# Kernel optimization log

Hardware: AMD Instinct MI355X
Metric: run time of the kernel (lower is better)

## Reference

```python
import jax, jax.numpy as jnp
import numpy as np

N, D_IN, D_OUT = 4096, 1024, 1024

def setup_inputs() -> dict:
    key = jax.random.key(0)
    k1, k2, k3, k4 = jax.random.split(key, 4)
    x = jax.random.normal(k1, (N, D_IN), dtype=jnp.float32)
    # original uses torch.rand (uniform [0,1)) for params
    w_query = jax.random.uniform(k2, (D_IN, D_OUT), dtype=jnp.float32)
    w_key = jax.random.uniform(k3, (D_IN, D_OUT), dtype=jnp.float32)
    w_value = jax.random.uniform(k4, (D_IN, D_OUT), dtype=jnp.float32)
    return {"x": x, "w_query": w_query, "w_key": w_key, "w_value": w_value}

def reference(x, w_query, w_key, w_value):
    queries = x @ w_query          # [N, d_out]
    keys = x @ w_key               # [N, d_out]
    values = x @ w_value           # [N, d_out]
    scale = keys.shape[-1] ** 0.5
    scores = queries @ keys.T      # [N, N]
    attn = jax.nn.softmax(scores / scale, axis=-1)
    return attn @ values           # [N, d_out]
```

## Files before the change

kernel.cpp:

```cpp
#include <hip/hip_runtime.h>
#include <math.h>

#define NROWS 4096
#define DDIM  1024

typedef __attribute__((ext_vector_type(8))) short short8;
typedef __attribute__((ext_vector_type(4))) float f32x4;

__device__ __forceinline__ ushort f2bf(float v) {
  union { float f; uint32_t u; } c; c.f = v;
  uint32_t u = c.u;
  uint32_t lsb = (u >> 16) & 1u;
  u += 0x7fffu + lsb;
  return (ushort)(u >> 16);
}
__device__ __forceinline__ float bf2f(ushort h) {
  union { uint32_t u; float f; } c; c.u = ((uint32_t)h) << 16;
  return c.f;
}

__device__ __forceinline__ void gll16(const void* g, void* l) {
  __builtin_amdgcn_global_load_lds((const __attribute__((address_space(1))) void*)g,
                                   (__attribute__((address_space(3))) void*)l, 16, 0, 0);
}

__device__ __forceinline__ size_t pidx(int r, int c, int ldt) {
  return ((size_t)((r >> 4) * ldt + (c >> 5))) * 512 +
         ((c >> 3) & 3) * 128 + (r & 15) * 8 + (c & 7);
}
__device__ __forceinline__ size_t pidxs(int r, int c, int ldt) {
  return ((size_t)((r >> 4) * ldt + (c >> 5))) * 1024 +
         ((c >> 3) & 3) * 128 + (r & 15) * 8 + (c & 7);
}

__global__ __launch_bounds__(256) void prep(const float* __restrict__ x,
                                            const float* __restrict__ wq,
                                            const float* __restrict__ wk,
                                            const float* __restrict__ wv,
                                            ushort* Xc,
                                            ushort* Wqc, ushort* Wkc, ushort* Wvh) {
  __shared__ float tl[32][33];
  const int b = blockIdx.x, t = threadIdx.x;
  if (b < 1024) {
    const f32x4* src = (const f32x4*)x;
#pragma unroll
    for (int r = 0; r < 4; ++r) {
      int i = b * 1024 + r * 256 + t;
      int row = i >> 8;
      int c = (i & 255) << 2;
      f32x4 v = __builtin_nontemporal_load(src + i);
      ushort4 h, l;
      h.x = f2bf(v.x); l.x = f2bf(v.x - bf2f(h.x));
      h.y = f2bf(v.y); l.y = f2bf(v.y - bf2f(h.y));
      h.z = f2bf(v.z); l.z = f2bf(v.z - bf2f(h.z));
      h.w = f2bf(v.w); l.w = f2bf(v.w - bf2f(h.w));
      size_t o = pidxs(row, c, DDIM / 32);
      *(ushort4*)(Xc + o) = h;
      *(ushort4*)(Xc + o + 512) = l;
    }
  } else {
    const int z = (b - 1024) >> 10;
    const int tile = (b - 1024) & 1023;
    const float* src = z == 0 ? wq : (z == 1 ? wk : wv);
    const int r0 = (tile >> 5) * 32;
    const int c0 = (tile & 31) * 32;
    const int tx = t & 31, ty = t >> 5;
    for (int i = ty; i < 32; i += 8)
      tl[i][tx] = __builtin_nontemporal_load(&src[(size_t)(r0 + i) * DDIM + c0 + tx]);
    __syncthreads();
    if (z == 2) {
      for (int i = ty; i < 32; i += 8) {
        float v = tl[tx][i];
        Wvh[pidx(c0 + i, r0 + tx, DDIM / 32)] = f2bf(v);
      }
    } else {
      ushort* d = z == 0 ? Wqc : Wkc;
      for (int i = ty; i < 32; i += 8) {
        float v = tl[tx][i];
        ushort h = f2bf(v);
        size_t o = pidxs(c0 + i, r0 + tx, DDIM / 32);
        d[o] = h;
        d[o + 512] = f2bf(v - bf2f(h));
      }
    }
  }
}

template <int MI, bool SPLIT, int KT, int SA, int SB>
__device__ __forceinline__ void direct_gemm(const ushort* __restrict__ A,
                                            const ushort* __restrict__ B,
                                            int m0, int n0, f32x4 (*acc)[4]) {
  const int t = threadIdx.x;
  const int wv = t >> 6, ln = t & 63;
  const int arb = (wv >> 1) * (MI * 16), crb = (wv & 1) * 64;
  const int ra = (m0 + arb) >> 4;
  const int rb = (n0 + crb) >> 4;

  uint oA[MI], oB[4];
#pragma unroll
  for (int i = 0; i < MI; ++i) oA[i] = (uint)(ra + i) * (uint)(KT * SA) + (uint)ln * 8u;
#pragma unroll
  for (int j = 0; j < 4; ++j) oB[j] = (uint)(rb + j) * (uint)(KT * SB) + (uint)ln * 8u;

  short8 ah0[MI], al0[MI], bh0[4], bl0[4];
  short8 ah1[MI], al1[MI], bh1[4], bl1[4];

#define DG_LOAD(sidx, AH, AL, BH, BL)                                        \
  {                                                                          \
    uint sa_ = (uint)(sidx) * (uint)SA;                                      \
    uint sb_ = (uint)(sidx) * (uint)SB;                                      \
    _Pragma("unroll") for (int i_ = 0; i_ < MI; ++i_) {                      \
      const ushort* pa_ = A + oA[i_] + sa_;                                  \
      AH[i_] = *(const short8*)pa_;                                          \
      if constexpr (SPLIT) AL[i_] = *(const short8*)(pa_ + 512);             \
    }                                                                        \
    _Pragma("unroll") for (int j_ = 0; j_ < 4; ++j_) {                       \
      const ushort* pb_ = B + oB[j_] + sb_;                                  \
      BH[j_] = *(const short8*)pb_;                                          \
      if constexpr (SPLIT) BL[j_] = *(const short8*)(pb_ + 512);             \
    }                                                                        \
  }

#define DG_MFMA(AH, AL, BH, BL)                                              \
  {                                                                          \
    __builtin_amdgcn_s_setprio(1);                                           \
    _Pragma("unroll") for (int j_ = 0; j_ < 4; ++j_) {                       \
      _Pragma("unroll") for (int i_ = 0; i_ < MI; ++i_) {                    \
        acc[i_][j_] = __builtin_amdgcn_mfma_f32_16x16x32_bf16(               \
            AH[i_], BH[j_], acc[i_][j_], 0, 0, 0);                           \
        if constexpr (SPLIT) {                                               \
          acc[i_][j_] = __builtin_amdgcn_mfma_f32_16x16x32_bf16(             \
              AH[i_], BL[j_], acc[i_][j_], 0, 0, 0);                         \
          acc[i_][j_] = __builtin_amdgcn_mfma_f32_16x16x32_bf16(             \
              AL[i_], BH[j_], acc[i_][j_], 0, 0, 0);                         \
        }                                                                    \
      }                                                                      \
    }                                                                        \
    __builtin_amdgcn_s_setprio(0);                                           \
  }

  DG_LOAD(0, ah0, al0, bh0, bl0);
#pragma unroll 1
  for (int s = 0; s < KT - 2; s += 2) {
    DG_LOAD(s + 1, ah1, al1, bh1, bl1);
    DG_MFMA(ah0, al0, bh0, bl0);
    DG_LOAD(s + 2, ah0, al0, bh0, bl0);
    DG_MFMA(ah1, al1, bh1, bl1);
  }
  DG_LOAD(KT - 1, ah1, al1, bh1, bl1);
  DG_MFMA(ah0, al0, bh0, bl0);
  DG_MFMA(ah1, al1, bh1, bl1);

#undef DG_LOAD
#undef DG_MFMA
}

__global__ __launch_bounds__(256) void gemm_qkv(const ushort* __restrict__ Xc,
                                                const ushort* __restrict__ Wqc,
                                                const ushort* __restrict__ Wkc,
                                                const ushort* __restrict__ Wvh,
                                                ushort* Qc, ushort* Kc, ushort* Vt) {
  const int id = blockIdx.y * 24 + blockIdx.x;
  const int wg = (id & 7) * 96 + (id >> 3);
  const int bx = wg % 24, by = wg / 24;
  const int which = bx % 3;
  const int g = bx / 3;
  const int t = threadIdx.x;
  const int wv = t >> 6, ln = t & 63;
  const int quad = ln >> 4, l16 = ln & 15;

  f32x4 acc[4][4];
#pragma unroll
  for (int i = 0; i < 4; ++i)
#pragma unroll
    for (int j = 0; j < 4; ++j) acc[i][j] = (f32x4){0.f, 0.f, 0.f, 0.f};

  if (which == 2) {
    const int m0 = g * 128;
    const int n0 = by * 128;
    direct_gemm<4, false, DDIM / 32, 512, 1024>(Wvh, Xc, m0, n0, acc);
#pragma unroll
    for (int i = 0; i < 4; ++i)
#pragma unroll
      for (int j = 0; j < 4; ++j) {
        int kv = n0 + (wv & 1) * 64 + j * 16 + l16;
        int d = m0 + (wv >> 1) * 64 + i * 16 + quad * 4;
#pragma unroll
        for (int r2 = 0; r2 < 4; ++r2)
          Vt[pidx(d + r2, kv, NROWS / 32)] = f2bf(acc[i][j][r2]);
      }
  } else {
    const int n0 = g * 128;
    const int m0 = by * 128;
    const ushort* Bc = which ? Wkc : Wqc;
    direct_gemm<4, true, DDIM / 32, 1024, 1024>(Xc, Bc, m0, n0, acc);
    const float scale = which ? 1.0f : 0.03125f;
    ushort* D = which ? Kc : Qc;
#pragma unroll
    for (int i = 0; i < 4; ++i)
#pragma unroll
      for (int j = 0; j < 4; ++j) {
        int col = n0 + (wv & 1) * 64 + j * 16 + l16;
        int rw = m0 + (wv >> 1) * 64 + i * 16 + quad * 4;
#pragma unroll
        for (int r2 = 0; r2 < 4; ++r2) {
          float v = acc[i][j][r2] * scale;
          ushort h = f2bf(v);
          size_t o = pidxs(rw + r2, col, DDIM / 32);
          D[o] = h;
          D[o + 512] = f2bf(v - bf2f(h));
        }
      }
  }
}

__global__ __launch_bounds__(512) void gemm_s(const ushort* __restrict__ Qc,
                                              const ushort* __restrict__ Kc,
                                              float* __restrict__ S) {
  __shared__ char smem[2][65536];
  const int bid = blockIdx.y * 16 + blockIdx.x;
  const int xcd = bid & 7, local = bid >> 3;
  const int m0 = ((xcd >> 1) * 4 + (local & 3)) * 256;
  const int n0 = ((xcd & 1) * 8 + (local >> 2)) * 256;
  const int t = threadIdx.x;
  const int w = t >> 6, ln = t & 63;
  const int wr = w >> 2, wc = w & 3;
  const int quad = ln >> 4, l16 = ln & 15;

  const char* srcBase = (w < 4)
      ? (const char*)Qc + (size_t)((m0 >> 4) + w * 4) * 65536
      : (const char*)Kc + (size_t)((n0 >> 4) + (w - 4) * 4) * 65536;
  srcBase += ln * 16;
  char* ldsBase = (char*)smem + w * 8192 + ln * 16;

  f32x4 acc[8][4];
#pragma unroll
  for (int i = 0; i < 8; ++i)
#pragma unroll
    for (int j = 0; j < 4; ++j) acc[i][j] = (f32x4){0.f, 0.f, 0.f, 0.f};

#pragma unroll
  for (int u = 0; u < 8; ++u)
    gll16(srcBase + (u >> 1) * 65536 + (u & 1) * 1024, ldsBase + u * 1024);
  asm volatile("s_waitcnt vmcnt(0)" ::: "memory");
  __builtin_amdgcn_s_barrier();

  const char* aB = (char*)smem + (wr * 8) * 2048 + ln * 16;
  const char* bB = (char*)smem + 32768 + (wc * 4) * 2048 + ln * 16;

#pragma unroll 1
  for (int kt = 0; kt < 32; ++kt) {
    const int cb = (kt & 1) << 16;
    const int nb = ((kt + 1) & 1) << 16;
    const char* srcK = srcBase + (size_t)(kt + 1) * 2048;

    if (kt < 31) {
#pragma unroll
      for (int u = 0; u < 8; ++u)
        gll16(srcK + (u >> 1) * 65536 + (u & 1) * 1024, ldsBase + nb + u * 1024);
    }

    short8 bh[4], bl[4];
#pragma unroll
    for (int j = 0; j < 4; ++j) {
      bh[j] = *(const short8*)(bB + cb + j * 2048);
      bl[j] = *(const short8*)(bB + cb + j * 2048 + 1024);
    }

#pragma unroll
    for (int p = 0; p < 4; ++p) {
      short8 ah0 = *(const short8*)(aB + cb + (2 * p) * 2048);
      short8 al0 = *(const short8*)(aB + cb + (2 * p) * 2048 + 1024);
      short8 ah1 = *(const short8*)(aB + cb + (2 * p + 1) * 2048);
      short8 al1 = *(const short8*)(aB + cb + (2 * p + 1) * 2048 + 1024);
      __builtin_amdgcn_s_setprio(1);
#pragma unroll
      for (int j_ = 0; j_ < 4; ++j_) {
        acc[2 * p][j_] = __builtin_amdgcn_mfma_f32_16x16x32_bf16(ah0, bh[j_], acc[2 * p][j_], 0, 0, 0);
        acc[2 * p][j_] = __builtin_amdgcn_mfma_f32_16x16x32_bf16(ah0, bl[j_], acc[2 * p][j_], 0, 0, 0);
        acc[2 * p][j_] = __builtin_amdgcn_mfma_f32_16x16x32_bf16(al0, bh[j_], acc[2 * p][j_], 0, 0, 0);
        acc[2 * p + 1][j_] = __builtin_amdgcn_mfma_f32_16x16x32_bf16(ah1, bh[j_], acc[2 * p + 1][j_], 0, 0, 0);
        acc[2 * p + 1][j_] = __builtin_amdgcn_mfma_f32_16x16x32_bf16(ah1, bl[j_], acc[2 * p + 1][j_], 0, 0, 0);
        acc[2 * p + 1][j_] = __builtin_amdgcn_mfma_f32_16x16x32_bf16(al1, bh[j_], acc[2 * p + 1][j_], 0, 0, 0);
      }
      __builtin_amdgcn_s_setprio(0);
    }

    asm volatile("s_waitcnt vmcnt(0)" ::: "memory");
    __builtin_amdgcn_s_barrier();
  }

#pragma unroll
  for (int i = 0; i < 8; ++i)
#pragma unroll
    for (int j = 0; j < 4; ++j) {
      int col = n0 + wc * 64 + j * 16 + l16;
      int rw = m0 + wr * 128 + i * 16 + quad * 4;
#pragma unroll
      for (int r2 = 0; r2 < 4; ++r2)
        S[(size_t)(rw + r2) * NROWS + col] = acc[i][j][r2];
    }
}

__global__ __launch_bounds__(256) void softmax_pack(const float* __restrict__ S,
                                                    ushort* __restrict__ P) {
  const int row = blockIdx.x, t = threadIdx.x;
  const float* Sr = S + (size_t)row * NROWS;
  const f32x4* S4 = (const f32x4*)Sr;
  f32x4 v[4];
  float mx = -3.4e38f;
#pragma unroll
  for (int c = 0; c < 4; ++c) {
    v[c] = S4[c * 256 + t];
    mx = fmaxf(mx, fmaxf(fmaxf(v[c].x, v[c].y), fmaxf(v[c].z, v[c].w)));
  }
  __shared__ float red[4];
  for (int o = 32; o >= 1; o >>= 1) mx = fmaxf(mx, __shfl_xor(mx, o));
  int wv = t >> 6, ln = t & 63;
  if (ln == 0) red[wv] = mx;
  __syncthreads();
  mx = fmaxf(fmaxf(red[0], red[1]), fmaxf(red[2], red[3]));
  float s = 0.f;
#pragma unroll
  for (int c = 0; c < 4; ++c) {
    v[c].x = __expf(v[c].x - mx);
    v[c].y = __expf(v[c].y - mx);
    v[c].z = __expf(v[c].z - mx);
    v[c].w = __expf(v[c].w - mx);
    s += v[c].x + v[c].y + v[c].z + v[c].w;
  }
  for (int o = 32; o >= 1; o >>= 1) s += __shfl_xor(s, o);
  __syncthreads();
  if (ln == 0) red[wv] = s;
  __syncthreads();
  s = red[0] + red[1] + red[2] + red[3];
  float inv = 1.f / s;
#pragma unroll
  for (int c = 0; c < 4; ++c) {
    ushort4 h;
    h.x = f2bf(v[c].x * inv);
    h.y = f2bf(v[c].y * inv);
    h.z = f2bf(v[c].z * inv);
    h.w = f2bf(v[c].w * inv);
    int c0 = 1024 * c + 4 * t;
    *(ushort4*)(P + pidx(row, c0, NROWS / 32)) = h;
  }
}

__global__ __launch_bounds__(256) void gemm_pv(const ushort* __restrict__ P,
                                               const ushort* __restrict__ Vt,
                                               float* __restrict__ Out) {
  const int n0 = blockIdx.x * 128, m0 = blockIdx.y * 128;
  const int t = threadIdx.x;
  const int wv = t >> 6, ln = t & 63;
  const int quad = ln >> 4, l16 = ln & 15;

  f32x4 acc[4][4];
#pragma unroll
  for (int i = 0; i < 4; ++i)
#pragma unroll
    for (int j = 0; j < 4; ++j) acc[i][j] = (f32x4){0.f, 0.f, 0.f, 0.f};

  direct_gemm<4, false, NROWS / 32, 512, 512>(P, Vt, m0, n0, acc);

#pragma unroll
  for (int i = 0; i < 4; ++i)
#pragma unroll
    for (int j = 0; j < 4; ++j) {
      int col = n0 + (wv & 1) * 64 + j * 16 + l16;
      int rw = m0 + (wv >> 1) * 64 + i * 16 + quad * 4;
#pragma unroll
      for (int r2 = 0; r2 < 4; ++r2)
        Out[(size_t)(rw + r2) * DDIM + col] = acc[i][j][r2];
    }
}

extern "C" void kernel_launch(void* const* d_in, const int* in_sizes, int n_in,
                              void* d_out, int out_size, void* d_ws, size_t ws_size,
                              hipStream_t stream) {
  const float* x  = (const float*)d_in[0];
  const float* wq = (const float*)d_in[1];
  const float* wk = (const float*)d_in[2];
  const float* wv = (const float*)d_in[3];
  char* ws = (char*)d_ws;
  const size_t MB = 1u << 20;

  ushort* Vt  = (ushort*)(ws + 0);
  ushort* Qc  = (ushort*)(ws + 8 * MB);
  ushort* Kc  = (ushort*)(ws + 24 * MB);
  ushort* Pp  = (ushort*)(ws + 8 * MB);
  ushort* Xc  = (ushort*)(ws + 40 * MB);
  ushort* Wqc = (ushort*)(ws + 56 * MB);
  ushort* Wkc = (ushort*)(ws + 60 * MB);
  ushort* Wvh = (ushort*)(ws + 64 * MB);
  float*  S   = (float*)(ws + 40 * MB);
  float*  Out = (float*)d_out;

  prep<<<4096, 256, 0, stream>>>(x, wq, wk, wv, Xc, Wqc, Wkc, Wvh);
  gemm_qkv<<<dim3(24, 32), 256, 0, stream>>>(Xc, Wqc, Wkc, Wvh, Qc, Kc, Vt);
  gemm_s<<<dim3(16, 16), 512, 0, stream>>>(Qc, Kc, S);
  softmax_pack<<<NROWS, 256, 0, stream>>>(S, Pp);
  gemm_pv<<<dim3(8, 32), 256, 0, stream>>>(Pp, Vt, Out);
}
```

Before: 314.6 us.

## Split-K the PV GEMM into two halves with a separate reduction kernel

The P·V GEMM grid gains a z-dimension of 2, so each block covers half of the 4096-long K dimension and writes fp32 partial outputs to two workspace buffers. A new reduce_add kernel then sums the partials into the output. direct_gemm gets a separate total-K stride parameter so a block can walk a K-subrange while row strides stay correct. This doubles the PV grid from 256 to 512 blocks to fill more compute units, at the cost of extra fp32 partial writes, one more kernel launch and an additional read pass.

```diff
diff --git a/kernel.cpp b/kernel.cpp
--- a/kernel.cpp
+++ b/kernel.cpp
@@ -86,7 +86,7 @@
   }
 }
 
-template <int MI, bool SPLIT, int KT, int SA, int SB>
+template <int MI, bool SPLIT, int KT, int KTOT, int SA, int SB>
 __device__ __forceinline__ void direct_gemm(const ushort* __restrict__ A,
                                             const ushort* __restrict__ B,
                                             int m0, int n0, f32x4 (*acc)[4]) {
@@ -98,9 +98,9 @@
 
   uint oA[MI], oB[4];
 #pragma unroll
-  for (int i = 0; i < MI; ++i) oA[i] = (uint)(ra + i) * (uint)(KT * SA) + (uint)ln * 8u;
-#pragma unroll
-  for (int j = 0; j < 4; ++j) oB[j] = (uint)(rb + j) * (uint)(KT * SB) + (uint)ln * 8u;
+  for (int i = 0; i < MI; ++i) oA[i] = (uint)(ra + i) * (uint)(KTOT * SA) + (uint)ln * 8u;
+#pragma unroll
+  for (int j = 0; j < 4; ++j) oB[j] = (uint)(rb + j) * (uint)(KTOT * SB) + (uint)ln * 8u;
 
   short8 ah0[MI], al0[MI], bh0[4], bl0[4];
   short8 ah1[MI], al1[MI], bh1[4], bl1[4];
@@ -178,7 +178,7 @@
   if (which == 2) {
     const int m0 = g * 128;
     const int n0 = by * 128;
-    direct_gemm<4, false, DDIM / 32, 512, 1024>(Wvh, Xc, m0, n0, acc);
+    direct_gemm<4, false, 32, 32, 512, 1024>(Wvh, Xc, m0, n0, acc);
 #pragma unroll
     for (int i = 0; i < 4; ++i)
 #pragma unroll
@@ -193,7 +193,7 @@
     const int n0 = g * 128;
     const int m0 = by * 128;
     const ushort* Bc = which ? Wkc : Wqc;
-    direct_gemm<4, true, DDIM / 32, 1024, 1024>(Xc, Bc, m0, n0, acc);
+    direct_gemm<4, true, 32, 32, 1024, 1024>(Xc, Bc, m0, n0, acc);
     const float scale = which ? 1.0f : 0.03125f;
     ushort* D = which ? Kc : Qc;
 #pragma unroll
@@ -349,8 +349,10 @@
 
 __global__ __launch_bounds__(256) void gemm_pv(const ushort* __restrict__ P,
                                                const ushort* __restrict__ Vt,
-                                               float* __restrict__ Out) {
+                                               float* __restrict__ Pa,
+                                               float* __restrict__ Pb) {
   const int n0 = blockIdx.x * 128, m0 = blockIdx.y * 128;
+  const int kb = blockIdx.z;
   const int t = threadIdx.x;
   const int wv = t >> 6, ln = t & 63;
   const int quad = ln >> 4, l16 = ln & 15;
@@ -361,8 +363,11 @@
 #pragma unroll
     for (int j = 0; j < 4; ++j) acc[i][j] = (f32x4){0.f, 0.f, 0.f, 0.f};
 
-  direct_gemm<4, false, NROWS / 32, 512, 512>(P, Vt, m0, n0, acc);
-
+  const ushort* Pk = P + (size_t)kb * 64 * 512;
+  const ushort* Vk = Vt + (size_t)kb * 64 * 512;
+  direct_gemm<4, false, 64, 128, 512, 512>(Pk, Vk, m0, n0, acc);
+
+  float* O = kb ? Pb : Pa;
 #pragma unroll
   for (int i = 0; i < 4; ++i)
 #pragma unroll
@@ -371,8 +376,20 @@
       int rw = m0 + (wv >> 1) * 64 + i * 16 + quad * 4;
 #pragma unroll
       for (int r2 = 0; r2 < 4; ++r2)
-        Out[(size_t)(rw + r2) * DDIM + col] = acc[i][j][r2];
-    }
+        O[(size_t)(rw + r2) * DDIM + col] = acc[i][j][r2];
+    }
+}
+
+__global__ __launch_bounds__(256) void reduce_add(const float* __restrict__ a,
+                                                  const float* __restrict__ b,
+                                                  float* __restrict__ out) {
+  size_t i = (size_t)blockIdx.x * 256 + threadIdx.x;
+  const f32x4* a4 = (const f32x4*)a;
+  const f32x4* b4 = (const f32x4*)b;
+  f32x4* o4 = (f32x4*)out;
+#pragma unroll
+  for (int r = 0; r < 2; ++r, i += (size_t)2048 * 256)
+    o4[i] = a4[i] + b4[i];
 }
 
 extern "C" void kernel_launch(void* const* d_in, const int* in_sizes, int n_in,
@@ -394,11 +411,14 @@
   ushort* Wkc = (ushort*)(ws + 60 * MB);
   ushort* Wvh = (ushort*)(ws + 64 * MB);
   float*  S   = (float*)(ws + 40 * MB);
+  float*  Pa  = (float*)(ws + 40 * MB);
+  float*  Pb  = (float*)(ws + 60 * MB);
   float*  Out = (float*)d_out;
 
   prep<<<4096, 256, 0, stream>>>(x, wq, wk, wv, Xc, Wqc, Wkc, Wvh);
   gemm_qkv<<<dim3(24, 32), 256, 0, stream>>>(Xc, Wqc, Wkc, Wvh, Qc, Kc, Vt);
   gemm_s<<<dim3(16, 16), 512, 0, stream>>>(Qc, Kc, S);
   softmax_pack<<<NROWS, 256, 0, stream>>>(S, Pp);
-  gemm_pv<<<dim3(8, 32), 256, 0, stream>>>(Pp, Vt, Out);
-}
+  gemm_pv<<<dim3(8, 32, 2), 256, 0, stream>>>(Pp, Vt, Pa, Pb);
+  reduce_add<<<2048, 256, 0, stream>>>(Pa, Pb, Out);
+}
```

New measurement: 327.3 us. +4.0%, slower.

## Switch QK^T score GEMM to 32x32x16 MFMA with 32-row packed layout

Applied to the files above, without the earlier changes.

Changes the Q/K packed layout to 32-row tiles and rewrites the score GEMM to use 32x32x16 bf16 MFMA with 4x2 f32x16 accumulators instead of 16x16x32 with 8x4. The larger MFMA shape cuts the number of LDS operand loads per FLOP and the instruction count. The direct_gemm template gains a KTOT parameter so the V and PV paths keep their old strides. It relies on the new layout staying consistent between the QKV projection store and the score GEMM loads, and it changes the output store pattern.

```diff
diff --git a/kernel.cpp b/kernel.cpp
--- a/kernel.cpp
+++ b/kernel.cpp
@@ -6,6 +6,7 @@
 
 typedef __attribute__((ext_vector_type(8))) short short8;
 typedef __attribute__((ext_vector_type(4))) float f32x4;
+typedef __attribute__((ext_vector_type(16))) float f32x16;
 
 __device__ __forceinline__ ushort f2bf(float v) {
   union { float f; uint32_t u; } c; c.f = v;
@@ -31,6 +32,10 @@
 __device__ __forceinline__ size_t pidxs(int r, int c, int ldt) {
   return ((size_t)((r >> 4) * ldt + (c >> 5))) * 1024 +
          ((c >> 3) & 3) * 128 + (r & 15) * 8 + (c & 7);
+}
+__device__ __forceinline__ size_t pidx32s(int r, int c, int ldt16) {
+  return ((size_t)((r >> 5) * ldt16 + (c >> 4))) * 1024 +
+         ((c >> 3) & 1) * 256 + (r & 31) * 8 + (c & 7);
 }
 
 __global__ __launch_bounds__(256) void prep(const float* __restrict__ x,
@@ -86,7 +91,7 @@
   }
 }
 
-template <int MI, bool SPLIT, int KT, int SA, int SB>
+template <int MI, bool SPLIT, int KT, int KTOT, int SA, int SB>
 __device__ __forceinline__ void direct_gemm(const ushort* __restrict__ A,
                                             const ushort* __restrict__ B,
                                             int m0, int n0, f32x4 (*acc)[4]) {
@@ -98,9 +103,9 @@
 
   uint oA[MI], oB[4];
 #pragma unroll
-  for (int i = 0; i < MI; ++i) oA[i] = (uint)(ra + i) * (uint)(KT * SA) + (uint)ln * 8u;
-#pragma unroll
-  for (int j = 0; j < 4; ++j) oB[j] = (uint)(rb + j) * (uint)(KT * SB) + (uint)ln * 8u;
+  for (int i = 0; i < MI; ++i) oA[i] = (uint)(ra + i) * (uint)(KTOT * SA) + (uint)ln * 8u;
+#pragma unroll
+  for (int j = 0; j < 4; ++j) oB[j] = (uint)(rb + j) * (uint)(KTOT * SB) + (uint)ln * 8u;
 
   short8 ah0[MI], al0[MI], bh0[4], bl0[4];
   short8 ah1[MI], al1[MI], bh1[4], bl1[4];
@@ -178,7 +183,7 @@
   if (which == 2) {
     const int m0 = g * 128;
     const int n0 = by * 128;
-    direct_gemm<4, false, DDIM / 32, 512, 1024>(Wvh, Xc, m0, n0, acc);
+    direct_gemm<4, false, 32, 32, 512, 1024>(Wvh, Xc, m0, n0, acc);
 #pragma unroll
     for (int i = 0; i < 4; ++i)
 #pragma unroll
@@ -193,7 +198,7 @@
     const int n0 = g * 128;
     const int m0 = by * 128;
     const ushort* Bc = which ? Wkc : Wqc;
-    direct_gemm<4, true, DDIM / 32, 1024, 1024>(Xc, Bc, m0, n0, acc);
+    direct_gemm<4, true, 32, 32, 1024, 1024>(Xc, Bc, m0, n0, acc);
     const float scale = which ? 1.0f : 0.03125f;
     ushort* D = which ? Kc : Qc;
 #pragma unroll
@@ -206,7 +211,7 @@
         for (int r2 = 0; r2 < 4; ++r2) {
           float v = acc[i][j][r2] * scale;
           ushort h = f2bf(v);
-          size_t o = pidxs(rw + r2, col, DDIM / 32);
+          size_t o = pidx32s(rw + r2, col, DDIM / 16);
           D[o] = h;
           D[o + 512] = f2bf(v - bf2f(h));
         }
@@ -225,63 +230,59 @@
   const int t = threadIdx.x;
   const int w = t >> 6, ln = t & 63;
   const int wr = w >> 2, wc = w & 3;
-  const int quad = ln >> 4, l16 = ln & 15;
 
   const char* srcBase = (w < 4)
-      ? (const char*)Qc + (size_t)((m0 >> 4) + w * 4) * 65536
-      : (const char*)Kc + (size_t)((n0 >> 4) + (w - 4) * 4) * 65536;
+      ? (const char*)Qc + (size_t)((m0 >> 5) + 2 * w) * 131072
+      : (const char*)Kc + (size_t)((n0 >> 5) + 2 * (w - 4)) * 131072;
   srcBase += ln * 16;
-  char* ldsBase = (char*)smem + w * 8192 + ln * 16;
-
-  f32x4 acc[8][4];
-#pragma unroll
-  for (int i = 0; i < 8; ++i)
-#pragma unroll
-    for (int j = 0; j < 4; ++j) acc[i][j] = (f32x4){0.f, 0.f, 0.f, 0.f};
+  char* ldsBase = (char*)smem + (w < 4 ? 0 : 32768) + (w & 3) * 8192 + ln * 16;
+
+  f32x16 acc[4][2];
+#pragma unroll
+  for (int i = 0; i < 4; ++i)
+#pragma unroll
+    for (int j = 0; j < 2; ++j) acc[i][j] = (f32x16)(0.f);
 
 #pragma unroll
   for (int u = 0; u < 8; ++u)
-    gll16(srcBase + (u >> 1) * 65536 + (u & 1) * 1024, ldsBase + u * 1024);
+    gll16(srcBase + (u >> 2) * 131072 + (u & 3) * 1024, ldsBase + u * 1024);
   asm volatile("s_waitcnt vmcnt(0)" ::: "memory");
   __builtin_amdgcn_s_barrier();
 
-  const char* aB = (char*)smem + (wr * 8) * 2048 + ln * 16;
-  const char* bB = (char*)smem + 32768 + (wc * 4) * 2048 + ln * 16;
+  const char* aB = (char*)smem + (wr * 4) * 4096 + ln * 16;
+  const char* bB = (char*)smem + 32768 + (wc * 2) * 4096 + ln * 16;
 
 #pragma unroll 1
   for (int kt = 0; kt < 32; ++kt) {
     const int cb = (kt & 1) << 16;
     const int nb = ((kt + 1) & 1) << 16;
-    const char* srcK = srcBase + (size_t)(kt + 1) * 2048;
+    const char* srcK = srcBase + (size_t)(kt + 1) * 4096;
 
     if (kt < 31) {
 #pragma unroll
       for (int u = 0; u < 8; ++u)
-        gll16(srcK + (u >> 1) * 65536 + (u & 1) * 1024, ldsBase + nb + u * 1024);
-    }
-
-    short8 bh[4], bl[4];
-#pragma unroll
-    for (int j = 0; j < 4; ++j) {
-      bh[j] = *(const short8*)(bB + cb + j * 2048);
-      bl[j] = *(const short8*)(bB + cb + j * 2048 + 1024);
-    }
-
-#pragma unroll
-    for (int p = 0; p < 4; ++p) {
-      short8 ah0 = *(const short8*)(aB + cb + (2 * p) * 2048);
-      short8 al0 = *(const short8*)(aB + cb + (2 * p) * 2048 + 1024);
-      short8 ah1 = *(const short8*)(aB + cb + (2 * p + 1) * 2048);
-      short8 al1 = *(const short8*)(aB + cb + (2 * p + 1) * 2048 + 1024);
+        gll16(srcK + (u >> 2) * 131072 + (u & 3) * 1024, ldsBase + nb + u * 1024);
+    }
+
+#pragma unroll
+    for (int ks = 0; ks < 2; ++ks) {
+      short8 bh[2], bl[2];
+#pragma unroll
+      for (int j = 0; j < 2; ++j) {
+        bh[j] = *(const short8*)(bB + cb + j * 4096 + ks * 2048);
+        bl[j] = *(const short8*)(bB + cb + j * 4096 + ks * 2048 + 1024);
+      }
       __builtin_amdgcn_s_setprio(1);
 #pragma unroll
-      for (int j_ = 0; j_ < 4; ++j_) {
-        acc[2 * p][j_] = __builtin_amdgcn_mfma_f32_16x16x32_bf16(ah0, bh[j_], acc[2 * p][j_], 0, 0, 0);
-        acc[2 * p][j_] = __builtin_amdgcn_mfma_f32_16x16x32_bf16(ah0, bl[j_], acc[2 * p][j_], 0, 0, 0);
-        acc[2 * p][j_] = __builtin_amdgcn_mfma_f32_16x16x32_bf16(al0, bh[j_], acc[2 * p][j_], 0, 0, 0);
-        acc[2 * p + 1][j_] = __builtin_amdgcn_mfma_f32_16x16x32_bf16(ah1, bh[j_], acc[2 * p + 1][j_], 0, 0, 0);
-        acc[2 * p + 1][j_] = __builtin_amdgcn_mfma_f32_16x16x32_bf16(ah1, bl[j_], acc[2 * p + 1][j_], 0, 0, 0);
-        acc[2 * p + 1][j_] = __builtin_amdgcn_mfma_f32_16x16x32_bf16(al1, bh[j_], acc[2 * p + 1][j_], 0, 0, 0);
+      for (int i = 0; i < 4; ++i) {
+        short8 ah = *(const short8*)(aB + cb + i * 4096 + ks * 2048);
+        short8 al = *(const short8*)(aB + cb + i * 4096 + ks * 2048 + 1024);
+#pragma unroll
+        for (int j = 0; j < 2; ++j) {
+          acc[i][j] = __builtin_amdgcn_mfma_f32_32x32x16_bf16(ah, bh[j], acc[i][j], 0, 0, 0);
+          acc[i][j] = __builtin_amdgcn_mfma_f32_32x32x16_bf16(ah, bl[j], acc[i][j], 0, 0, 0);
+          acc[i][j] = __builtin_amdgcn_mfma_f32_32x32x16_bf16(al, bh[j], acc[i][j], 0, 0, 0);
+        }
       }
       __builtin_amdgcn_s_setprio(0);
     }
@@ -291,14 +292,16 @@
   }
 
 #pragma unroll
-  for (int i = 0; i < 8; ++i)
-#pragma unroll
-    for (int j = 0; j < 4; ++j) {
-      int col = n0 + wc * 64 + j * 16 + l16;
-      int rw = m0 + wr * 128 + i * 16 + quad * 4;
-#pragma unroll
-      for (int r2 = 0; r2 < 4; ++r2)
-        S[(size_t)(rw + r2) * NROWS + col] = acc[i][j][r2];
+  for (int i = 0; i < 4; ++i)
+#pragma unroll
+    for (int j = 0; j < 2; ++j) {
+      int colb = n0 + wc * 64 + j * 32 + (ln & 31);
+      int rowb = m0 + wr * 128 + i * 32 + ((ln >> 5) << 2);
+#pragma unroll
+      for (int reg = 0; reg < 16; ++reg) {
+        int row = rowb + (reg & 3) + ((reg >> 2) << 3);
+        S[(size_t)row * NROWS + colb] = acc[i][j][reg];
+      }
     }
 }
 
@@ -361,7 +364,7 @@
 #pragma unroll
     for (int j = 0; j < 4; ++j) acc[i][j] = (f32x4){0.f, 0.f, 0.f, 0.f};
 
-  direct_gemm<4, false, NROWS / 32, 512, 512>(P, Vt, m0, n0, acc);
+  direct_gemm<4, false, 128, 128, 512, 512>(P, Vt, m0, n0, acc);
 
 #pragma unroll
   for (int i = 0; i < 4; ++i)
```

Result: slower. 325.1 us (+3.3%).

## Stage QKV GEMM tiles through double-buffered LDS with direct global-to-LDS loads

Applied to the files above, without the earlier changes.

The QKV projection kernel now streams A/B tiles into a double-buffered LDS region using global_load_lds, then feeds MFMAs from LDS, where it used to load operands directly from global memory into registers. It also remaps block indices into XCD-grouped tiles to improve L2 locality, and raises wave priority around the MFMA section. The direct_gemm template gains a separate total-K parameter for the PV kernel, which keeps the same values. The change is meant to cut redundant global traffic and latency stalls in the QKV GEMM, in exchange for 64KB of LDS per block and a barrier on every k-step.

```diff
diff --git a/kernel.cpp b/kernel.cpp
--- a/kernel.cpp
+++ b/kernel.cpp
@@ -86,7 +86,7 @@
   }
 }
 
-template <int MI, bool SPLIT, int KT, int SA, int SB>
+template <int MI, bool SPLIT, int KT, int KTOT, int SA, int SB>
 __device__ __forceinline__ void direct_gemm(const ushort* __restrict__ A,
                                             const ushort* __restrict__ B,
                                             int m0, int n0, f32x4 (*acc)[4]) {
@@ -98,9 +98,9 @@
 
   uint oA[MI], oB[4];
 #pragma unroll
-  for (int i = 0; i < MI; ++i) oA[i] = (uint)(ra + i) * (uint)(KT * SA) + (uint)ln * 8u;
-#pragma unroll
-  for (int j = 0; j < 4; ++j) oB[j] = (uint)(rb + j) * (uint)(KT * SB) + (uint)ln * 8u;
+  for (int i = 0; i < MI; ++i) oA[i] = (uint)(ra + i) * (uint)(KTOT * SA) + (uint)ln * 8u;
+#pragma unroll
+  for (int j = 0; j < 4; ++j) oB[j] = (uint)(rb + j) * (uint)(KTOT * SB) + (uint)ln * 8u;
 
   short8 ah0[MI], al0[MI], bh0[4], bl0[4];
   short8 ah1[MI], al1[MI], bh1[4], bl1[4];
@@ -160,13 +160,14 @@
                                                 const ushort* __restrict__ Wkc,
                                                 const ushort* __restrict__ Wvh,
                                                 ushort* Qc, ushort* Kc, ushort* Vt) {
-  const int id = blockIdx.y * 24 + blockIdx.x;
-  const int wg = (id & 7) * 96 + (id >> 3);
-  const int bx = wg % 24, by = wg / 24;
-  const int which = bx % 3;
-  const int g = bx / 3;
+  __shared__ char smem[2][32768];
+  const int bid = blockIdx.x;
+  const int which = bid >> 8;
+  const int local = bid & 255;
+  const int xcd = local & 7, idx = local >> 3;
   const int t = threadIdx.x;
-  const int wv = t >> 6, ln = t & 63;
+  const int w = t >> 6, ln = t & 63;
+  const int wr = w >> 1, wc = w & 1;
   const int quad = ln >> 4, l16 = ln & 15;
 
   f32x4 acc[4][4];
@@ -175,33 +176,68 @@
 #pragma unroll
     for (int j = 0; j < 4; ++j) acc[i][j] = (f32x4){0.f, 0.f, 0.f, 0.f};
 
-  if (which == 2) {
-    const int m0 = g * 128;
-    const int n0 = by * 128;
-    direct_gemm<4, false, DDIM / 32, 512, 1024>(Wvh, Xc, m0, n0, acc);
-#pragma unroll
-    for (int i = 0; i < 4; ++i)
+  if (which < 2) {
+    const int m0 = (xcd * 4 + (idx >> 3)) * 128;
+    const int n0 = (idx & 7) * 128;
+    const ushort* Bc = which ? Wkc : Wqc;
+    const char* srcBase = (w < 2)
+        ? (const char*)Xc + (size_t)((m0 >> 4) + (w & 1) * 4) * 65536
+        : (const char*)Bc + (size_t)((n0 >> 4) + (w & 1) * 4) * 65536;
+    srcBase += ln * 16;
+    char* ldsBase = (char*)smem + (w < 2 ? 0 : 16384) + (w & 1) * 8192 + ln * 16;
+
+#pragma unroll
+    for (int u = 0; u < 8; ++u)
+      gll16(srcBase + (u >> 1) * 65536 + (u & 1) * 1024, ldsBase + u * 1024);
+    asm volatile("s_waitcnt vmcnt(0)" ::: "memory");
+    __builtin_amdgcn_s_barrier();
+
+    const char* aB = (char*)smem + wr * 8192 + ln * 16;
+    const char* bB = (char*)smem + 16384 + wc * 8192 + ln * 16;
+
+#pragma unroll 1
+    for (int kt = 0; kt < 32; ++kt) {
+      const int cb = (kt & 1) << 15;
+      const int nb = ((kt + 1) & 1) << 15;
+      if (kt < 31) {
+        const char* srcK = srcBase + (size_t)(kt + 1) * 2048;
+#pragma unroll
+        for (int u = 0; u < 8; ++u)
+          gll16(srcK + (u >> 1) * 65536 + (u & 1) * 1024, ldsBase + nb + u * 1024);
+      }
+
+      short8 bh[4], bl[4];
 #pragma unroll
       for (int j = 0; j < 4; ++j) {
-        int kv = n0 + (wv & 1) * 64 + j * 16 + l16;
-        int d = m0 + (wv >> 1) * 64 + i * 16 + quad * 4;
-#pragma unroll
-        for (int r2 = 0; r2 < 4; ++r2)
-          Vt[pidx(d + r2, kv, NROWS / 32)] = f2bf(acc[i][j][r2]);
-      }
-  } else {
-    const int n0 = g * 128;
-    const int m0 = by * 128;
-    const ushort* Bc = which ? Wkc : Wqc;
-    direct_gemm<4, true, DDIM / 32, 1024, 1024>(Xc, Bc, m0, n0, acc);
+        bh[j] = *(const short8*)(bB + cb + j * 2048);
+        bl[j] = *(const short8*)(bB + cb + j * 2048 + 1024);
+      }
+      __builtin_amdgcn_s_setprio(1);
+#pragma unroll
+      for (int i = 0; i < 4; ++i) {
+        short8 ah = *(const short8*)(aB + cb + i * 2048);
+        short8 al = *(const short8*)(aB + cb + i * 2048 + 1024);
+#pragma unroll
+        for (int j = 0; j < 4; ++j) {
+          acc[i][j] = __builtin_amdgcn_mfma_f32_16x16x32_bf16(ah, bh[j], acc[i][j], 0, 0, 0);
+          acc[i][j] = __builtin_amdgcn_mfma_f32_16x16x32_bf16(ah, bl[j], acc[i][j], 0, 0, 0);
+          acc[i][j] = __builtin_amdgcn_mfma_f32_16x16x32_bf16(al, bh[j], acc[i][j], 0, 0, 0);
+        }
+      }
+      __builtin_amdgcn_s_setprio(0);
+
+      asm volatile("s_waitcnt vmcnt(0)" ::: "memory");
+      __builtin_amdgcn_s_barrier();
+    }
+
     const float scale = which ? 1.0f : 0.03125f;
     ushort* D = which ? Kc : Qc;
 #pragma unroll
     for (int i = 0; i < 4; ++i)
 #pragma unroll
       for (int j = 0; j < 4; ++j) {
-        int col = n0 + (wv & 1) * 64 + j * 16 + l16;
-        int rw = m0 + (wv >> 1) * 64 + i * 16 + quad * 4;
+        int col = n0 + wc * 64 + j * 16 + l16;
+        int rw = m0 + wr * 64 + i * 16 + quad * 4;
 #pragma unroll
         for (int r2 = 0; r2 < 4; ++r2) {
           float v = acc[i][j][r2] * scale;
@@ -210,6 +246,65 @@
           D[o] = h;
           D[o + 512] = f2bf(v - bf2f(h));
         }
+      }
+  } else {
+    const int m0 = (idx & 7) * 128;
+    const int n0 = (xcd * 4 + (idx >> 3)) * 128;
+    const char* srcBase = (w < 2)
+        ? (const char*)Wvh + (size_t)((m0 >> 4) + (w & 1) * 4) * 32768
+        : (const char*)Xc + (size_t)((n0 >> 4) + (w & 1) * 4) * 65536;
+    srcBase += ln * 16;
+    char* ldsBase = (char*)smem + (w < 2 ? 0 : 8192) + (w & 1) * 4096 + ln * 16;
+    const size_t srcStep = (w < 2) ? 1024 : 2048;
+    const size_t rowStr = (w < 2) ? 32768 : 65536;
+
+#pragma unroll
+    for (int u = 0; u < 4; ++u)
+      gll16(srcBase + (size_t)u * rowStr, ldsBase + u * 1024);
+    asm volatile("s_waitcnt vmcnt(0)" ::: "memory");
+    __builtin_amdgcn_s_barrier();
+
+    const char* aB = (char*)smem + wr * 4096 + ln * 16;
+    const char* bB = (char*)smem + 8192 + wc * 4096 + ln * 16;
+
+#pragma unroll 1
+    for (int kt = 0; kt < 32; ++kt) {
+      const int cb = (kt & 1) << 15;
+      const int nb = ((kt + 1) & 1) << 15;
+      if (kt < 31) {
+        const char* srcK = srcBase + (size_t)(kt + 1) * srcStep;
+#pragma unroll
+        for (int u = 0; u < 4; ++u)
+          gll16(srcK + (size_t)u * rowStr, ldsBase + nb + u * 1024);
+      }
+
+      short8 bh[4];
+#pragma unroll
+      for (int j = 0; j < 4; ++j)
+        bh[j] = *(const short8*)(bB + cb + j * 1024);
+      __builtin_amdgcn_s_setprio(1);
+#pragma unroll
+      for (int i = 0; i < 4; ++i) {
+        short8 ah = *(const short8*)(aB + cb + i * 1024);
+#pragma unroll
+        for (int j = 0; j < 4; ++j)
+          acc[i][j] = __builtin_amdgcn_mfma_f32_16x16x32_bf16(ah, bh[j], acc[i][j], 0, 0, 0);
+      }
+      __builtin_amdgcn_s_setprio(0);
+
+      asm volatile("s_waitcnt vmcnt(0)" ::: "memory");
+      __builtin_amdgcn_s_barrier();
+    }
+
+#pragma unroll
+    for (int i = 0; i < 4; ++i)
+#pragma unroll
+      for (int j = 0; j < 4; ++j) {
+        int kv = n0 + wc * 64 + j * 16 + l16;
+        int d = m0 + wr * 64 + i * 16 + quad * 4;
+#pragma unroll
+        for (int r2 = 0; r2 < 4; ++r2)
+          Vt[pidx(d + r2, kv, NROWS / 32)] = f2bf(acc[i][j][r2]);
       }
   }
 }
@@ -361,7 +456,7 @@
 #pragma unroll
     for (int j = 0; j < 4; ++j) acc[i][j] = (f32x4){0.f, 0.f, 0.f, 0.f};
 
-  direct_gemm<4, false, NROWS / 32, 512, 512>(P, Vt, m0, n0, acc);
+  direct_gemm<4, false, 128, 128, 512, 512>(P, Vt, m0, n0, acc);
 
 #pragma unroll
   for (int i = 0; i < 4; ++i)
@@ -397,7 +492,7 @@
   float*  Out = (float*)d_out;
 
   prep<<<4096, 256, 0, stream>>>(x, wq, wk, wv, Xc, Wqc, Wkc, Wvh);
-  gemm_qkv<<<dim3(24, 32), 256, 0, stream>>>(Xc, Wqc, Wkc, Wvh, Qc, Kc, Vt);
+  gemm_qkv<<<768, 256, 0, stream>>>(Xc, Wqc, Wkc, Wvh, Qc, Kc, Vt);
   gemm_s<<<dim3(16, 16), 512, 0, stream>>>(Qc, Kc, S);
   softmax_pack<<<NROWS, 256, 0, stream>>>(S, Pp);
   gemm_pv<<<dim3(8, 32), 256, 0, stream>>>(Pp, Vt, Out);
```

Measured after the change: 300.5 us. 4.5% less time.
